# Kernel optimization log

Hardware: AMD Instinct MI355X
Metric: run time of the kernel (lower is better)

Reference implementation:

```python
import jax, jax.numpy as jnp
import numpy as np

B = 512
SHAPE = (64, 64, 64)   # mode dims I1,I2,I3
RANKS = (8, 8, 8)      # Tucker ranks R1,R2,R3
SEP = 4                # separation rank (number of Tucker terms)


def setup_inputs() -> dict:
    key = jax.random.key(0)
    k_x, k_core, k_fac = jax.random.split(key, 3)
    x = jax.random.normal(k_x, (B,) + SHAPE, dtype=jnp.float32)
    core = jax.random.normal(k_core, RANKS, dtype=jnp.float32)
    # factors[s, k] is the mode-k factor matrix [I_k, R_k] of term s
    factors = jax.random.normal(k_fac, (SEP, len(SHAPE), SHAPE[0], RANKS[0]), dtype=jnp.float32)
    return {"x": x, "core": core, "factors": factors}


def reference(x, core, factors):
    # expand_to_tensor: sum_s multi_mode_dot(core, factors[s])
    # T[i,j,k] = sum_s sum_abc core[a,b,c] * U1_s[i,a] * U2_s[j,b] * U3_s[k,c]
    T = jnp.einsum('abc,sia,sjb,skc->ijk',
                   core, factors[:, 0], factors[:, 1], factors[:, 2])
    # tenalg.inner(x, T, n_modes=order): contract the last `order` modes -> [B]
    return jnp.einsum('bijk,ijk->b', x, T)
```

## Files before the change

kernel.cpp:

```cpp
#include <hip/hip_runtime.h>
#include <hip/hip_bf16.h>


typedef float fvec4 __attribute__((ext_vector_type(4)));

__global__ __launch_bounds__(256) void tucker_expand_kernel(
    const float* __restrict__ core,
    const float* __restrict__ factors,
    float* __restrict__ T) {
  const int i = blockIdx.x;
  const int t = threadIdx.x;

  __shared__ float core_s[512];
  __shared__ float c1[64];
  __shared__ float c2[512];
  __shared__ float u3[64 * 9];

  core_s[t]       = core[t];
  core_s[t + 256] = core[t + 256];

  float tacc[16];
#pragma unroll
  for (int m = 0; m < 16; ++m) tacc[m] = 0.f;

  for (int s = 0; s < 4; ++s) {
    {
      const float* U3 = factors + ((s * 3 + 2) * 64) * 8;
      int e0 = t, e1 = t + 256;
      u3[(e0 >> 3) * 9 + (e0 & 7)] = U3[e0];
      u3[(e1 >> 3) * 9 + (e1 & 7)] = U3[e1];
    }
    __syncthreads();

    if (t < 64) {
      const float* U1row = factors + ((s * 3 + 0) * 64 + i) * 8;
      float v = 0.f;
#pragma unroll
      for (int a = 0; a < 8; ++a) v += core_s[a * 64 + t] * U1row[a];
      c1[t] = v;
    }
    __syncthreads();

    {
      const float* U2 = factors + ((s * 3 + 1) * 64) * 8;
#pragma unroll
      for (int rep = 0; rep < 2; ++rep) {
        int e = t + rep * 256;
        int j = e >> 3, c = e & 7;
        float v = 0.f;
#pragma unroll
        for (int b = 0; b < 8; ++b) v += U2[j * 8 + b] * c1[b * 8 + c];
        c2[e] = v;
      }
    }
    __syncthreads();

#pragma unroll
    for (int m = 0; m < 16; ++m) {
      int e = m * 256 + t;
      int j = e >> 6, k = e & 63;
      float v = 0.f;
#pragma unroll
      for (int c = 0; c < 8; ++c) v += u3[k * 9 + c] * c2[j * 8 + c];
      tacc[m] += v;
    }
    __syncthreads();
  }

#pragma unroll
  for (int m = 0; m < 16; ++m) T[i * 4096 + m * 256 + t] = tacc[m];
}

__global__ __launch_bounds__(1024, 8) void dot_kernel(
    const float* __restrict__ x,
    const float* __restrict__ T,
    float* __restrict__ out) {
  const int b = blockIdx.x;
  const int t = threadIdx.x;

  const fvec4* x4 = reinterpret_cast<const fvec4*>(x + (size_t)b * 262144);
  const fvec4* t4 = reinterpret_cast<const fvec4*>(T);

  float a0 = 0.f, a1 = 0.f, a2 = 0.f, a3 = 0.f;
#pragma unroll 4
  for (int i = 0; i < 64; ++i) {
    int idx = i * 1024 + t;
    fvec4 xv = __builtin_nontemporal_load(x4 + idx);
    fvec4 tv = t4[idx];
    a0 += xv.x * tv.x;
    a1 += xv.y * tv.y;
    a2 += xv.z * tv.z;
    a3 += xv.w * tv.w;
  }
  float sum = (a0 + a1) + (a2 + a3);

#pragma unroll
  for (int off = 32; off > 0; off >>= 1) sum += __shfl_down(sum, off, 64);

  __shared__ float wsum[16];
  const int wave = t >> 6, lane = t & 63;
  if (lane == 0) wsum[wave] = sum;
  __syncthreads();
  if (wave == 0) {
    float v = (lane < 16) ? wsum[lane] : 0.f;
    v += __shfl_down(v, 8, 64);
    v += __shfl_down(v, 4, 64);
    v += __shfl_down(v, 2, 64);
    v += __shfl_down(v, 1, 64);
    if (lane == 0) out[b] = v;
  }
}

extern "C" void kernel_launch(void* const* d_in, const int* in_sizes, int n_in,
                              void* d_out, int out_size, void* d_ws, size_t ws_size,
                              hipStream_t stream) {
  const float* x       = (const float*)d_in[0];
  const float* core    = (const float*)d_in[1];
  const float* factors = (const float*)d_in[2];
  float* out = (float*)d_out;

  float* T = (float*)d_ws;

  tucker_expand_kernel<<<64, 256, 0, stream>>>(core, factors, T);
  dot_kernel<<<512, 1024, 0, stream>>>(x, T, out);
}
```

Measured before the change: 670.4 us.

## Split batch dot product into slab-partitioned blocks with LDS-staged T and two-stage reduction

The single 512-block dot kernel becomes 8192 blocks of 256 threads. Each block handles one of 32 slabs of T, stages that slab in LDS and applies it to two batch items, writing per-slab partial sums that a small second kernel reduces. The aim is more blocks in flight for the bandwidth-bound read of x, and less re-reading of T from cache. The cost is an extra kernel launch and partial-sum traffic, with an atomic fallback path used when workspace is too small.

```diff
diff --git a/kernel.cpp b/kernel.cpp
--- a/kernel.cpp
+++ b/kernel.cpp
@@ -71,44 +71,119 @@
   for (int m = 0; m < 16; ++m) T[i * 4096 + m * 256 + t] = tacc[m];
 }
 
-__global__ __launch_bounds__(1024, 8) void dot_kernel(
+__global__ __launch_bounds__(256) void dot_stage1(
+    const float* __restrict__ x,
+    const float* __restrict__ T,
+    float* __restrict__ partial) {
+  const int blk = blockIdx.x;
+  const int s   = blk & 31;
+  const int bp  = blk >> 5;
+  const int tid = threadIdx.x;
+
+  __shared__ fvec4 Tl[2048];
+
+  const fvec4* tg = reinterpret_cast<const fvec4*>(T) + s * 2048;
+#pragma unroll
+  for (int k = 0; k < 8; ++k) Tl[k * 256 + tid] = tg[k * 256 + tid];
+  __syncthreads();
+
+  const fvec4* xg0 =
+      reinterpret_cast<const fvec4*>(x) + (size_t)(bp * 2) * 65536 + s * 2048;
+  const fvec4* xg1 = xg0 + 65536;
+
+  float a0 = 0.f, a1 = 0.f, a2 = 0.f, a3 = 0.f;
+  float c0 = 0.f, c1 = 0.f, c2 = 0.f, c3 = 0.f;
+#pragma unroll
+  for (int k = 0; k < 8; ++k) {
+    fvec4 xv0 = __builtin_nontemporal_load(xg0 + k * 256 + tid);
+    fvec4 xv1 = __builtin_nontemporal_load(xg1 + k * 256 + tid);
+    fvec4 tv  = Tl[k * 256 + tid];
+    a0 += xv0.x * tv.x; a1 += xv0.y * tv.y;
+    a2 += xv0.z * tv.z; a3 += xv0.w * tv.w;
+    c0 += xv1.x * tv.x; c1 += xv1.y * tv.y;
+    c2 += xv1.z * tv.z; c3 += xv1.w * tv.w;
+  }
+  float s0 = (a0 + a1) + (a2 + a3);
+  float s1 = (c0 + c1) + (c2 + c3);
+
+#pragma unroll
+  for (int off = 32; off > 0; off >>= 1) {
+    s0 += __shfl_down(s0, off, 64);
+    s1 += __shfl_down(s1, off, 64);
+  }
+
+  __syncthreads();
+  float* red = reinterpret_cast<float*>(Tl);
+  const int wave = tid >> 6, lane = tid & 63;
+  if (lane == 0) { red[wave] = s0; red[4 + wave] = s1; }
+  __syncthreads();
+  if (tid == 0) {
+    partial[s * 512 + bp * 2]     = (red[0] + red[1]) + (red[2] + red[3]);
+    partial[s * 512 + bp * 2 + 1] = (red[4] + red[5]) + (red[6] + red[7]);
+  }
+}
+
+__global__ __launch_bounds__(512) void zero_out(float* __restrict__ out) {
+  out[threadIdx.x] = 0.f;
+}
+
+__global__ __launch_bounds__(256) void dot_stage1_atomic(
     const float* __restrict__ x,
     const float* __restrict__ T,
     float* __restrict__ out) {
-  const int b = blockIdx.x;
-  const int t = threadIdx.x;
-
-  const fvec4* x4 = reinterpret_cast<const fvec4*>(x + (size_t)b * 262144);
-  const fvec4* t4 = reinterpret_cast<const fvec4*>(T);
+  const int blk = blockIdx.x;
+  const int s   = blk & 31;
+  const int bp  = blk >> 5;
+  const int tid = threadIdx.x;
+
+  __shared__ fvec4 Tl[2048];
+  const fvec4* tg = reinterpret_cast<const fvec4*>(T) + s * 2048;
+#pragma unroll
+  for (int k = 0; k < 8; ++k) Tl[k * 256 + tid] = tg[k * 256 + tid];
+  __syncthreads();
+
+  const fvec4* xg0 =
+      reinterpret_cast<const fvec4*>(x) + (size_t)(bp * 2) * 65536 + s * 2048;
+  const fvec4* xg1 = xg0 + 65536;
 
   float a0 = 0.f, a1 = 0.f, a2 = 0.f, a3 = 0.f;
-#pragma unroll 4
-  for (int i = 0; i < 64; ++i) {
-    int idx = i * 1024 + t;
-    fvec4 xv = __builtin_nontemporal_load(x4 + idx);
-    fvec4 tv = t4[idx];
-    a0 += xv.x * tv.x;
-    a1 += xv.y * tv.y;
-    a2 += xv.z * tv.z;
-    a3 += xv.w * tv.w;
-  }
-  float sum = (a0 + a1) + (a2 + a3);
-
-#pragma unroll
-  for (int off = 32; off > 0; off >>= 1) sum += __shfl_down(sum, off, 64);
-
-  __shared__ float wsum[16];
-  const int wave = t >> 6, lane = t & 63;
-  if (lane == 0) wsum[wave] = sum;
-  __syncthreads();
-  if (wave == 0) {
-    float v = (lane < 16) ? wsum[lane] : 0.f;
-    v += __shfl_down(v, 8, 64);
-    v += __shfl_down(v, 4, 64);
-    v += __shfl_down(v, 2, 64);
-    v += __shfl_down(v, 1, 64);
-    if (lane == 0) out[b] = v;
-  }
+  float c0 = 0.f, c1 = 0.f, c2 = 0.f, c3 = 0.f;
+#pragma unroll
+  for (int k = 0; k < 8; ++k) {
+    fvec4 xv0 = __builtin_nontemporal_load(xg0 + k * 256 + tid);
+    fvec4 xv1 = __builtin_nontemporal_load(xg1 + k * 256 + tid);
+    fvec4 tv  = Tl[k * 256 + tid];
+    a0 += xv0.x * tv.x; a1 += xv0.y * tv.y;
+    a2 += xv0.z * tv.z; a3 += xv0.w * tv.w;
+    c0 += xv1.x * tv.x; c1 += xv1.y * tv.y;
+    c2 += xv1.z * tv.z; c3 += xv1.w * tv.w;
+  }
+  float s0 = (a0 + a1) + (a2 + a3);
+  float s1 = (c0 + c1) + (c2 + c3);
+#pragma unroll
+  for (int off = 32; off > 0; off >>= 1) {
+    s0 += __shfl_down(s0, off, 64);
+    s1 += __shfl_down(s1, off, 64);
+  }
+  __syncthreads();
+  float* red = reinterpret_cast<float*>(Tl);
+  const int wave = tid >> 6, lane = tid & 63;
+  if (lane == 0) { red[wave] = s0; red[4 + wave] = s1; }
+  __syncthreads();
+  if (tid == 0) {
+    atomicAdd(&out[bp * 2],     (red[0] + red[1]) + (red[2] + red[3]));
+    atomicAdd(&out[bp * 2 + 1], (red[4] + red[5]) + (red[6] + red[7]));
+  }
+}
+
+__global__ __launch_bounds__(64) void dot_stage2(
+    const float* __restrict__ partial,
+    float* __restrict__ out) {
+  const int b = blockIdx.x * 64 + threadIdx.x;
+  float v = 0.f;
+#pragma unroll
+  for (int s = 0; s < 32; ++s) v += partial[s * 512 + b];
+  out[b] = v;
 }
 
 extern "C" void kernel_launch(void* const* d_in, const int* in_sizes, int n_in,
@@ -122,5 +197,14 @@
   float* T = (float*)d_ws;
 
   tucker_expand_kernel<<<64, 256, 0, stream>>>(core, factors, T);
-  dot_kernel<<<512, 1024, 0, stream>>>(x, T, out);
-}
+
+  const size_t need = (size_t)(262144 + 32 * 512) * sizeof(float);
+  if (ws_size >= need) {
+    float* partial = T + 262144;
+    dot_stage1<<<8192, 256, 0, stream>>>(x, T, partial);
+    dot_stage2<<<8, 64, 0, stream>>>(partial, out);
+  } else {
+    zero_out<<<1, 512, 0, stream>>>(out);
+    dot_stage1_atomic<<<8192, 256, 0, stream>>>(x, T, out);
+  }
+}
```

Measured after the change: 648.4 us. 3.3% less time.
